# Kernel tuning notes

Measured on AMD Instinct MI355X. Metric: run time of the kernel, lower is better.

Reference implementation:

```python
import jax, jax.numpy as jnp
import numpy as np

K = 5            # self.k
MARGIN_CB = 0.05  # neighborhood_ranking_crossbrain default margin
MARGIN_NRC = 0.4  # self.margin used in partial_nrc_loss
MAX_PAIRS = 6
EPS = 1e-8


def _norm(x):
    return x / jnp.sqrt(jnp.sum(x * x, axis=-1, keepdims=True) + 1e-12)


def _cos_dist_pair(a, b):
    s = jnp.clip(jnp.sum(a * b, axis=-1), -1.0 + EPS, 1.0 - EPS)
    return 1.0 - s


def _pairwise_cos_dist(x, y):
    return 1.0 - _norm(x) @ _norm(y).T


def _sq_dist(x):
    # squared euclidean distance -- same argsort order as torch.cdist
    sq = jnp.sum(x * x, axis=-1)
    return jnp.maximum(sq[:, None] + sq[None, :] - 2.0 * (x @ x.T), 0.0)


def _crossbrain(z1, z2, key):
    # neighborhood_ranking_crossbrain with match_idx = identity (as in forward)
    N = z1.shape[0]
    D1 = jax.lax.stop_gradient(_sq_dist(z1))      # ranking only, no grad
    neigh = jnp.argsort(D1, axis=-1)[:, 1:K + 1]  # (N, K) nearest neighbors
    # sample K distinct negatives per token excluding {n} U neigh[n]:
    scores = jax.random.uniform(key, (N, N))
    rows = jnp.arange(N)
    scores = scores.at[rows[:, None], neigh].set(-jnp.inf)
    scores = scores.at[rows, rows].set(-jnp.inf)
    _, neg = jax.lax.top_k(scores, K)             # (N, K)
    z2n = _norm(z2)
    anchor = z2n[:, None, :]                      # (N,1,C)
    d_pos = _cos_dist_pair(anchor, z2n[neigh])    # (N, K)
    d_neg = _cos_dist_pair(anchor, z2n[neg])      # (N, K)
    return jnp.mean(jax.nn.relu(d_pos - d_neg + MARGIN_CB))


def _nrc_partial(A, B, key):
    # partial_matches_mnn + nrc_on_partial, fully vectorized & masked
    T = A.shape[0]
    D = jax.lax.stop_gradient(_pairwise_cos_dist(A, B))
    b_of_a = jnp.argmin(D, axis=1)
    a_of_b = jnp.argmin(D, axis=0)
    ar = jnp.arange(T)
    mutual = ar == a_of_b[b_of_a]                 # matched A tokens (injective)
    idxB_of_A = jnp.where(mutual, b_of_a, -1)
    is_matched_B = (jnp.zeros(T, jnp.int32).at[b_of_a].add(mutual.astype(jnp.int32)) > 0)
    DA = jax.lax.stop_gradient(_pairwise_cos_dist(A, A))
    neigh = jnp.argsort(DA, axis=-1)[:, 1:K + 1]  # (T, K)
    DB = _pairwise_cos_dist(B, B)                 # grads flow through DB
    posB = idxB_of_A[neigh]                       # (T, K)
    pos_mask = posB >= 0
    # negative pool: unmatched B tokens (stable argsort puts False first)
    order = jnp.argsort(is_matched_B)
    neg_count = jnp.maximum(T - jnp.sum(is_matched_B.astype(jnp.int32)), 1)
    r = jax.random.randint(key, (T, K), 0, T)
    negB = order[r % neg_count]                   # sample with replacement
    uB = jnp.maximum(idxB_of_A, 0)[:, None]
    d_pos = DB[uB, jnp.maximum(posB, 0)]
    d_neg = DB[uB, negB]
    hinge = jax.nn.relu(d_pos - d_neg + MARGIN_NRC) * pos_mask
    per_tok = jnp.sum(hinge, axis=1) / jnp.maximum(jnp.sum(pos_mask, axis=1), 1)
    valid = mutual & jnp.any(pos_mask, axis=1)
    cnt = jnp.sum(valid.astype(jnp.float32))
    return jnp.where(cnt > 0, jnp.sum(per_tok * valid) / jnp.maximum(cnt, 1.0), 0.0)


def _partial_nrc_loss(z1, z2, key, seed):
    Bn = z1.shape[0]
    pairs = [(p, q) for p in range(Bn) for q in range(Bn) if p != q]
    rng = np.random.RandomState(seed)
    if len(pairs) > MAX_PAIRS:
        sel = rng.permutation(len(pairs))[:MAX_PAIRS]
        pairs = [pairs[i] for i in sel]
    ps = jnp.array([p for p, _ in pairs])
    qs = jnp.array([q for _, q in pairs])
    keys = jax.random.split(key, len(pairs))
    losses = jax.vmap(_nrc_partial)(z1[ps], z2[qs], keys)
    return jnp.mean(losses)


def _taco_loss(z1, z2):
    Bn = z1.shape[0]
    base = jax.random.key(42)
    k1, k2, k3, k4 = jax.random.split(base, 4)
    loss2 = (jnp.sum(jax.vmap(_crossbrain)(z1, z2, jax.random.split(k1, Bn)))
             + jnp.sum(jax.vmap(_crossbrain)(z2, z1, jax.random.split(k2, Bn)))) / Bn
    loss3 = _partial_nrc_loss(z1, z2, k3, 0) + _partial_nrc_loss(z2, z1, k4, 1)
    return 10.0 * loss2 + 10.0 * loss3


def setup_inputs() -> dict:
    key = jax.random.key(0)
    k1, k2 = jax.random.split(key)
    Bn, T, C = 4, 2048, 768
    z1 = jax.random.normal(k1, (Bn, T, C), dtype=jnp.float32)
    z2 = jax.random.normal(k2, (Bn, T, C), dtype=jnp.float32)
    return {"z1": z1, "z2": z2}


def reference(z1, z2):
    return _taco_loss(z1, z2)
```

## Files before the change

### kernel.cpp

```cpp
#include <hip/hip_runtime.h>
#include <cstdint>
#include <cstddef>

#define TT 2048
#define CC 768
#define KK 5
#define PCAP 64

typedef __attribute__((ext_vector_type(8))) short short8;
typedef __attribute__((ext_vector_type(4))) short short4v;
typedef __attribute__((ext_vector_type(4))) float float4v;

struct PairTab { int sa[12]; int sb[12]; };
struct PairMap { int src[12]; int tr[12]; };

#define N_SELF_BLK (8 * 136)
#define TP 132

__device__ __forceinline__ unsigned int mix_hash(unsigned int a, unsigned int b) {
  unsigned long long x = (((unsigned long long)a) << 32) | (unsigned long long)b;
  x ^= x >> 33; x *= 0xff51afd7ed558ccdULL;
  x ^= x >> 33; x *= 0xc4ceb9fe1a85ec53ULL;
  x ^= x >> 33;
  return (unsigned int)(x & 0xffffffffu);
}

__device__ __forceinline__ unsigned short f2bf(float x) {
  union { float f; unsigned int u; } v; v.f = x;
  unsigned int r = v.u + 0x7fffu + ((v.u >> 16) & 1u);
  return (unsigned short)(r >> 16);
}

__device__ __forceinline__ float bf2f(unsigned short u) {
  union { unsigned int i; float f; } v; v.i = ((unsigned int)u) << 16; return v.f;
}

__device__ __forceinline__ void gload_lds16(const void* g, void* l) {
  __builtin_amdgcn_global_load_lds(
      (const __attribute__((address_space(1))) unsigned int*)g,
      (__attribute__((address_space(3))) unsigned int*)l, 16, 0, 0);
}

__device__ __forceinline__ bool lexlt(float k1, int i1, float k2, int i2) {
  return k1 < k2 || (k1 == k2 && i1 < i2);
}

#define INS5(kk_, ii_, L)                                                        \
  if (lexlt(kk_, ii_, L##k[4], L##i[4])) {                                       \
    L##k[4] = kk_; L##i[4] = ii_;                                                \
    if (lexlt(L##k[4], L##i[4], L##k[3], L##i[3])) {                             \
      float tk = L##k[3]; int ti_ = L##i[3]; L##k[3] = L##k[4]; L##i[3] = L##i[4]; L##k[4] = tk; L##i[4] = ti_; \
      if (lexlt(L##k[3], L##i[3], L##k[2], L##i[2])) {                           \
        tk = L##k[2]; ti_ = L##i[2]; L##k[2] = L##k[3]; L##i[2] = L##i[3]; L##k[3] = tk; L##i[3] = ti_; \
        if (lexlt(L##k[2], L##i[2], L##k[1], L##i[1])) {                         \
          tk = L##k[1]; ti_ = L##i[1]; L##k[1] = L##k[2]; L##i[1] = L##i[2]; L##k[2] = tk; L##i[2] = ti_; \
          if (lexlt(L##k[1], L##i[1], L##k[0], L##i[0])) {                       \
            tk = L##k[0]; ti_ = L##i[0]; L##k[0] = L##k[1]; L##i[0] = L##i[1]; L##k[1] = tk; L##i[1] = ti_; \
          }                                                                      \
        }                                                                        \
      }                                                                          \
    }                                                                            \
  }

__global__ __launch_bounds__(192) void prep_kernel(const float* __restrict__ z1, const float* __restrict__ z2,
                                                   unsigned short* __restrict__ zb, float* __restrict__ sq,
                                                   float* __restrict__ inv) {
  int r = blockIdx.x;
  const float* p = (r < 4 * TT) ? (z1 + (size_t)r * CC) : (z2 + (size_t)(r - 4 * TT) * CC);
  unsigned short* o = zb + (size_t)r * CC;
  float4 v = ((const float4*)p)[threadIdx.x];
  float s = v.x * v.x + v.y * v.y + v.z * v.z + v.w * v.w;
  ushort4 u;
  u.x = f2bf(v.x); u.y = f2bf(v.y); u.z = f2bf(v.z); u.w = f2bf(v.w);
  ((ushort4*)o)[threadIdx.x] = u;
#pragma unroll
  for (int off = 32; off > 0; off >>= 1) s += __shfl_down(s, off, 64);
  __shared__ float wred[3];
  int lane = threadIdx.x & 63, w = threadIdx.x >> 6;
  if (lane == 0) wred[w] = s;
  __syncthreads();
  if (threadIdx.x == 0) {
    float tot = wred[0] + wred[1] + wred[2];
    sq[r] = tot; inv[r] = rsqrtf(tot + 1e-12f);
  }
}

struct SmemKL { unsigned short As[128 * 64]; unsigned short Bs[128 * 64]; };
union SmemU {
  SmemKL st;
  unsigned short tile[128 * TP];
};

__device__ __forceinline__ void gram_mainloop(const unsigned short* __restrict__ A,
                                              const unsigned short* __restrict__ B,
                                              int bm, int bn, SmemKL& st, float4v (&acc)[4][4]) {
  const int lane = threadIdx.x & 63, waveId = threadIdx.x >> 6;
  const int wm = (waveId >> 1) * 64, wn = (waveId & 1) * 64;
  const int lrow = lane & 15, lquad = lane >> 4;
  for (int kk = 0; kk < CC; kk += 64) {
#pragma unroll
    for (int c = 0; c < 4; ++c) {
      int l = c * 256 + threadIdx.x;
      int row = l >> 3, pc = l & 7;
      int sc = pc ^ (row & 7);
      gload_lds16(A + (size_t)(bm + row) * CC + kk + sc * 8, &st.As[l * 8]);
      gload_lds16(B + (size_t)(bn + row) * CC + kk + sc * 8, &st.Bs[l * 8]);
    }
    __syncthreads();
#pragma unroll
    for (int h = 0; h < 2; ++h) {
      short8 af[4], bfr[4];
#pragma unroll
      for (int i = 0; i < 4; ++i) {
        int ra = wm + i * 16 + lrow;
        int ca = (h * 4 + lquad) ^ (ra & 7);
        af[i] = *(const short8*)&st.As[ra * 64 + ca * 8];
        int rb = wn + i * 16 + lrow;
        int cb2 = (h * 4 + lquad) ^ (rb & 7);
        bfr[i] = *(const short8*)&st.Bs[rb * 64 + cb2 * 8];
      }
#pragma unroll
      for (int i = 0; i < 4; ++i)
#pragma unroll
        for (int j = 0; j < 4; ++j)
          acc[i][j] = __builtin_amdgcn_mfma_f32_16x16x32_bf16(af[i], bfr[j], acc[i][j], 0, 0, 0);
    }
    __syncthreads();
  }
}

__global__ __launch_bounds__(256, 4) void gram_self(const unsigned short* __restrict__ zb,
                                                    unsigned short* __restrict__ gram) {
  __shared__ SmemU sm;
  const int bid = blockIdx.x;
  int s = bid / 136;
  int t = bid % 136;
  int ti = 0;
  while (t >= 16 - ti) { t -= 16 - ti; ++ti; }
  int tj = ti + t;
  int bm = ti * 128, bn = tj * 128;
  const unsigned short* A = zb + (size_t)s * TT * CC;

  float4v acc[4][4];
#pragma unroll
  for (int i = 0; i < 4; ++i)
#pragma unroll
    for (int j = 0; j < 4; ++j) acc[i][j] = (float4v){0.f, 0.f, 0.f, 0.f};

  gram_mainloop(A, A, bm, bn, sm.st, acc);

  const int lane = threadIdx.x & 63, waveId = threadIdx.x >> 6;
  const int wm = (waveId >> 1) * 64, wn = (waveId & 1) * 64;
  const int lrow = lane & 15, lquad = lane >> 4;

#pragma unroll
  for (int i = 0; i < 4; ++i)
#pragma unroll
    for (int j = 0; j < 4; ++j)
#pragma unroll
      for (int r = 0; r < 4; ++r) {
        int lr = wm + i * 16 + lquad * 4 + r;
        int lc = wn + j * 16 + lrow;
        sm.tile[lr * TP + lc] = f2bf(acc[i][j][r]);
      }
  __syncthreads();
  unsigned short* G = gram + (size_t)s * TT * TT;
  for (int it = 0; it < 16; ++it) {
    int task = it * 256 + threadIdx.x;
    int r = task >> 5;
    int c = task & 31;
    short4v v = *(const short4v*)&sm.tile[r * TP + c * 4];
    *(short4v*)&G[(size_t)(bm + r) * TT + bn + c * 4] = v;
  }
  if (bm != bn) {
    for (int it = 0; it < 16; ++it) {
      int task = it * 256 + threadIdx.x;
      int cc = task >> 5;
      int q = task & 31;
      short4v v;
      v[0] = (short)sm.tile[(q * 4 + 0) * TP + cc];
      v[1] = (short)sm.tile[(q * 4 + 1) * TP + cc];
      v[2] = (short)sm.tile[(q * 4 + 2) * TP + cc];
      v[3] = (short)sm.tile[(q * 4 + 3) * TP + cc];
      *(short4v*)&G[(size_t)(bn + cc) * TT + bm + q * 4] = v;
    }
  }
}

__global__ __launch_bounds__(256, 4) void gram_cross(const unsigned short* __restrict__ zb,
                                                     const float* __restrict__ invAll, PairTab tab,
                                                     float* __restrict__ prow_v, int* __restrict__ prow_i,
                                                     float* __restrict__ pcol_v, int* __restrict__ pcol_i) {
  __shared__ SmemKL smk;
  __shared__ float sInvA[128], sInvB[128];
  __shared__ float rowv[2][128]; __shared__ int rowi[2][128];
  __shared__ float colv[2][128]; __shared__ int coli[2][128];

  const int cbid = blockIdx.x;
  const int p = cbid >> 8;
  const int tile = cbid & 255;
  const int bn = (tile & 15) * 128;
  const int bm = (tile >> 4) * 128;
  const unsigned short* A = zb + (size_t)tab.sa[p] * TT * CC;
  const unsigned short* B = zb + (size_t)tab.sb[p] * TT * CC;
  if (threadIdx.x < 128) sInvA[threadIdx.x] = invAll[(size_t)tab.sa[p] * TT + bm + threadIdx.x];
  else sInvB[threadIdx.x - 128] = invAll[(size_t)tab.sb[p] * TT + bn + threadIdx.x - 128];

  float4v acc[4][4];
#pragma unroll
  for (int i = 0; i < 4; ++i)
#pragma unroll
    for (int j = 0; j < 4; ++j) acc[i][j] = (float4v){0.f, 0.f, 0.f, 0.f};

  gram_mainloop(A, B, bm, bn, smk, acc);

  const int lane = threadIdx.x & 63, waveId = threadIdx.x >> 6;
  const int wm = (waveId >> 1) * 64, wn = (waveId & 1) * 64;
  const int lrow = lane & 15, lquad = lane >> 4;

  float rbv[4][4]; int rbi[4][4];
#pragma unroll
  for (int i = 0; i < 4; ++i)
#pragma unroll
    for (int r = 0; r < 4; ++r) { rbv[i][r] = INFINITY; rbi[i][r] = TT; }
#pragma unroll
  for (int i = 0; i < 4; ++i)
#pragma unroll
    for (int j = 0; j < 4; ++j) {
      int col = bn + wn + j * 16 + lrow;
      float ivb = sInvB[wn + j * 16 + lrow];
#pragma unroll
      for (int r = 0; r < 4; ++r) {
        float v = -acc[i][j][r] * ivb;
        if (v < rbv[i][r]) { rbv[i][r] = v; rbi[i][r] = col; }
      }
    }
#pragma unroll
  for (int m = 1; m <= 8; m <<= 1) {
#pragma unroll
    for (int i = 0; i < 4; ++i)
#pragma unroll
      for (int r = 0; r < 4; ++r) {
        float v2 = __shfl_xor(rbv[i][r], m, 64);
        int i2 = __shfl_xor(rbi[i][r], m, 64);
        if (v2 < rbv[i][r] || (v2 == rbv[i][r] && i2 < rbi[i][r])) { rbv[i][r] = v2; rbi[i][r] = i2; }
      }
  }
  if (lrow == 0) {
#pragma unroll
    for (int i = 0; i < 4; ++i)
#pragma unroll
      for (int r = 0; r < 4; ++r) {
        int lr = wm + i * 16 + lquad * 4 + r;
        rowv[wn >> 6][lr] = rbv[i][r]; rowi[wn >> 6][lr] = rbi[i][r];
      }
  }

  float cbv[4]; int cbi[4];
#pragma unroll
  for (int j = 0; j < 4; ++j) { cbv[j] = INFINITY; cbi[j] = TT; }
#pragma unroll
  for (int j = 0; j < 4; ++j)
#pragma unroll
    for (int i = 0; i < 4; ++i)
#pragma unroll
      for (int r = 0; r < 4; ++r) {
        int lr = wm + i * 16 + lquad * 4 + r;
        float v = -acc[i][j][r] * sInvA[lr];
        if (v < cbv[j]) { cbv[j] = v; cbi[j] = bm + lr; }
      }
#pragma unroll
  for (int m = 16; m <= 32; m <<= 1) {
#pragma unroll
    for (int j = 0; j < 4; ++j) {
      float v2 = __shfl_xor(cbv[j], m, 64);
      int i2 = __shfl_xor(cbi[j], m, 64);
      if (v2 < cbv[j] || (v2 == cbv[j] && i2 < cbi[j])) { cbv[j] = v2; cbi[j] = i2; }
    }
  }
  if (lquad == 0) {
#pragma unroll
    for (int j = 0; j < 4; ++j) {
      int lc = wn + j * 16 + lrow;
      colv[wm >> 6][lc] = cbv[j]; coli[wm >> 6][lc] = cbi[j];
    }
  }
  __syncthreads();

  int bj = bn >> 7, bi2 = bm >> 7;
  if (threadIdx.x < 128) {
    int t = threadIdx.x;
    float v0 = rowv[0][t], v1 = rowv[1][t];
    int i0 = rowi[0][t], i1 = rowi[1][t];
    bool take1 = (v1 < v0) || (v1 == v0 && i1 < i0);
    prow_v[((size_t)p * 16 + bj) * TT + bm + t] = take1 ? v1 : v0;
    prow_i[((size_t)p * 16 + bj) * TT + bm + t] = take1 ? i1 : i0;
  } else {
    int t = threadIdx.x - 128;
    float v0 = colv[0][t], v1 = colv[1][t];
    int i0 = coli[0][t], i1 = coli[1][t];
    bool take1 = (v1 < v0) || (v1 == v0 && i1 < i0);
    pcol_v[((size_t)p * 16 + bi2) * TT + bn + t] = take1 ? v1 : v0;
    pcol_i[((size_t)p * 16 + bi2) * TT + bn + t] = take1 ? i1 : i0;
  }
}

__device__ void top5_row_full(const unsigned short* __restrict__ G, const float* __restrict__ sq,
                              const float* __restrict__ inv, int i, int lane,
                              int* __restrict__ o0, int* __restrict__ o1) {
  float ak[5]; int ai[5];
  float bk[5]; int bi[5];
#pragma unroll
  for (int t = 0; t < 5; ++t) { ak[t] = INFINITY; ai[t] = TT; bk[t] = INFINITY; bi[t] = TT; }
#pragma unroll
  for (int step = 0; step < 8; ++step) {
    int j4 = (step * 64 + lane) * 4;
    ushort4 g4u = *(const ushort4*)&G[j4];
    float4 s4 = *(const float4*)&sq[j4];
    float4 v4 = *(const float4*)&inv[j4];
#pragma unroll
    for (int c = 0; c < 4; ++c) {
      int j = j4 + c;
      float g = bf2f((c == 0) ? g4u.x : (c == 1) ? g4u.y : (c == 2) ? g4u.z : g4u.w);
      float sv = (c == 0) ? s4.x : (c == 1) ? s4.y : (c == 2) ? s4.z : s4.w;
      float iv = (c == 0) ? v4.x : (c == 1) ? v4.y : (c == 2) ? v4.z : v4.w;
      float k0 = (j == i) ? INFINITY : sv - 2.f * g;
      float k1 = (j == i) ? INFINITY : -g * iv;
      INS5(k0, j, a)
      INS5(k1, j, b)
    }
  }
#pragma unroll
  for (int m = 1; m <= 32; m <<= 1) {
    float ok[5]; int oi[5];
#pragma unroll
    for (int t = 0; t < 5; ++t) { ok[t] = __shfl_xor(ak[t], m, 64); oi[t] = __shfl_xor(ai[t], m, 64); }
#pragma unroll
    for (int t = 0; t < 5; ++t) { INS5(ok[t], oi[t], a) }
#pragma unroll
    for (int t = 0; t < 5; ++t) { ok[t] = __shfl_xor(bk[t], m, 64); oi[t] = __shfl_xor(bi[t], m, 64); }
#pragma unroll
    for (int t = 0; t < 5; ++t) { INS5(ok[t], oi[t], b) }
  }
  if (lane < KK) {
    int v0 = (lane == 0) ? ai[0] : (lane == 1) ? ai[1] : (lane == 2) ? ai[2] : (lane == 3) ? ai[3] : ai[4];
    int v1 = (lane == 0) ? bi[0] : (lane == 1) ? bi[1] : (lane == 2) ? bi[2] : (lane == 3) ? bi[3] : bi[4];
    o0[lane] = v0;
    o1[lane] = v1;
  }
}

__global__ __launch_bounds__(256) void top5_batched(const unsigned short* __restrict__ gram,
                                                    const float* __restrict__ sqAll,
                                                    const float* __restrict__ invAll,
                                                    int* __restrict__ out0, int* __restrict__ out1) {
  int s = blockIdx.y;
  int w = threadIdx.x >> 6, lane = threadIdx.x & 63;
  int i = blockIdx.x * 4 + w;
  const unsigned short* G = gram + (size_t)s * TT * TT + (size_t)i * TT;
  const float* sq = sqAll + (size_t)s * TT;
  const float* inv = invAll + (size_t)s * TT;

  __shared__ float pvv[4][2][PCAP];
  __shared__ int pix[4][2][PCAP];
  __shared__ int pcnt[4][2];
  if (lane < 2) pcnt[w][lane] = 0;

  float mn0 = INFINITY, mn1 = INFINITY;
#pragma unroll
  for (int step = 0; step < 8; ++step) {
    int j4 = (step * 64 + lane) * 4;
    ushort4 g4u = *(const ushort4*)&G[j4];
    float4 s4 = *(const float4*)&sq[j4];
    float4 v4 = *(const float4*)&inv[j4];
#pragma unroll
    for (int c = 0; c < 4; ++c) {
      int j = j4 + c;
      float g = bf2f((c == 0) ? g4u.x : (c == 1) ? g4u.y : (c == 2) ? g4u.z : g4u.w);
      float sv = (c == 0) ? s4.x : (c == 1) ? s4.y : (c == 2) ? s4.z : s4.w;
      float iv = (c == 0) ? v4.x : (c == 1) ? v4.y : (c == 2) ? v4.z : v4.w;
      float k0 = (j == i) ? INFINITY : sv - 2.f * g;
      float k1 = (j == i) ? INFINITY : -g * iv;
      mn0 = fminf(mn0, k0);
      mn1 = fminf(mn1, k1);
    }
  }
#pragma unroll
  for (int m = 1; m <= 4; m <<= 1) {
    mn0 = fminf(mn0, __shfl_xor(mn0, m, 64));
    mn1 = fminf(mn1, __shfl_xor(mn1, m, 64));
  }
  float gv0[8], gv1[8];
#pragma unroll
  for (int g = 0; g < 8; ++g) {
    gv0[g] = __shfl(mn0, g * 8, 64);
    gv1[g] = __shfl(mn1, g * 8, 64);
  }
  float T0 = 0.f, T1 = 0.f;
#pragma unroll
  for (int g = 0; g < 8; ++g) {
    int r0 = 0, r1 = 0;
#pragma unroll
    for (int h = 0; h < 8; ++h) {
      r0 += ((gv0[h] < gv0[g]) || (gv0[h] == gv0[g] && h < g)) ? 1 : 0;
      r1 += ((gv1[h] < gv1[g]) || (gv1[h] == gv1[g] && h < g)) ? 1 : 0;
    }
    if (r0 == 4) T0 = gv0[g];
    if (r1 == 4) T1 = gv1[g];
  }

#pragma unroll
  for (int step = 0; step < 8; ++step) {
    int j4 = (step * 64 + lane) * 4;
    ushort4 g4u = *(const ushort4*)&G[j4];
    float4 s4 = *(const float4*)&sq[j4];
    float4 v4 = *(const float4*)&inv[j4];
#pragma unroll
    for (int c = 0; c < 4; ++c) {
      int j = j4 + c;
      float g = bf2f((c == 0) ? g4u.x : (c == 1) ? g4u.y : (c == 2) ? g4u.z : g4u.w);
      float sv = (c == 0) ? s4.x : (c == 1) ? s4.y : (c == 2) ? s4.z : s4.w;
      float iv = (c == 0) ? v4.x : (c == 1) ? v4.y : (c == 2) ? v4.z : v4.w;
      float k0 = (j == i) ? INFINITY : sv - 2.f * g;
      float k1 = (j == i) ? INFINITY : -g * iv;
      bool c0 = (k0 <= T0), c1 = (k1 <= T1);
      if (__any(c0)) {
        if (c0) {
          int q = atomicAdd(&pcnt[w][0], 1);
          if (q < PCAP) { pvv[w][0][q] = k0; pix[w][0][q] = j; }
        }
      }
      if (__any(c1)) {
        if (c1) {
          int q = atomicAdd(&pcnt[w][1], 1);
          if (q < PCAP) { pvv[w][1][q] = k1; pix[w][1][q] = j; }
        }
      }
    }
  }

  int c0n = pcnt[w][0], c1n = pcnt[w][1];
  if (c0n > PCAP || c1n > PCAP) {
    top5_row_full(G, sq, inv, i, lane,
                  out0 + ((size_t)s * TT + i) * KK, out1 + ((size_t)s * TT + i) * KK);
    return;
  }
  {
    float cv = (lane < c0n) ? pvv[w][0][lane] : INFINITY;
    int ci = (lane < c0n) ? pix[w][0][lane] : TT;
    int r = 0;
    for (int t = 0; t < c0n; ++t) {
      float ov = pvv[w][0][t]; int oi = pix[w][0][t];
      r += lexlt(ov, oi, cv, ci) ? 1 : 0;
    }
    if (lane < c0n && r < KK) out0[((size_t)s * TT + i) * KK + r] = ci;
  }
  {
    float cv = (lane < c1n) ? pvv[w][1][lane] : INFINITY;
    int ci = (lane < c1n) ? pix[w][1][lane] : TT;
    int r = 0;
    for (int t = 0; t < c1n; ++t) {
      float ov = pvv[w][1][t]; int oi = pix[w][1][t];
      r += lexlt(ov, oi, cv, ci) ? 1 : 0;
    }
    if (lane < c1n && r < KK) out1[((size_t)s * TT + i) * KK + r] = ci;
  }
}

__device__ void argmin_body(int bx, int p, const float* __restrict__ prow_v, const int* __restrict__ prow_i,
                            const float* __restrict__ pcol_v, const int* __restrict__ pcol_i,
                            const PairMap& pm,
                            int* __restrict__ b_of_a, int* __restrict__ a_of_b) {
  int u = pm.src[p];
  bool tr = pm.tr[p] != 0;
  int t = bx * 256 + threadIdx.x;
  int isRow = t < TT;
  int x = isRow ? t : t - TT;
  bool useRow = (isRow != 0) != tr;
  const float* pv = (useRow ? prow_v : pcol_v) + (size_t)u * 16 * TT;
  const int* pi = (useRow ? prow_i : pcol_i) + (size_t)u * 16 * TT;
  float best = INFINITY; int bidx = TT;
  for (int s = 0; s < 16; ++s) {
    float v = pv[(size_t)s * TT + x]; int id = pi[(size_t)s * TT + x];
    if (v < best || (v == best && id < bidx)) { best = v; bidx = id; }
  }
  if (isRow) b_of_a[(size_t)p * TT + x] = bidx;
  else       a_of_b[(size_t)p * TT + x] = bidx;
}

__device__ void cb_hinge_body(int bx, int c, const unsigned short* __restrict__ gram, const float* __restrict__ invAll,
                              const int* __restrict__ neigh1, float* __restrict__ cb_acc) {
  int i0 = bx * 64;
  int sa = c, sb = (c < 4) ? (c + 4) : (c - 4);
  const unsigned short* Gs = gram + (size_t)sb * TT * TT;
  const float* invB = invAll + (size_t)sb * TT;
  const int* neighA = neigh1 + (size_t)sa * TT * KK;
  unsigned int seed = 0x13579BDFu + 0x9E3779B9u * (unsigned)c;
  int tid = threadIdx.x;

  __shared__ int targ[64][10];
  __shared__ float sval[64][10];
  for (int t = tid; t < 64 * KK; t += 256) targ[t / KK][t % KK] = neighA[(size_t)i0 * KK + t];
  __syncthreads();
  if (tid < 64) {
    int i = i0 + tid;
    int pos[KK];
#pragma unroll
    for (int k = 0; k < KK; ++k) pos[k] = targ[tid][k];
    unsigned int ctr = 0;
    for (int k = 0; k < KK; ++k) {
      int cand;
      while (true) {
        unsigned int h = mix_hash(seed ^ (unsigned)i, ctr++);
        cand = (int)(h & (TT - 1));
        bool bad = (cand == i);
        for (int t = 0; t < KK; ++t) bad = bad || (cand == pos[t]);
        for (int t = 0; t < k; ++t) bad = bad || (cand == targ[tid][KK + t]);
        if (!bad) break;
      }
      targ[tid][KK + k] = cand;
    }
  }
  __syncthreads();
  for (int t = tid; t < 640; t += 256) {
    int il = t / 10, k = t % 10;
    int tt = targ[il][k];
    sval[il][k] = bf2f(Gs[(size_t)(i0 + il) * TT + tt]) * invB[tt];
  }
  __syncthreads();
  if (tid < 64) {
    int i = i0 + tid;
    float ii = invB[i];
    const float lo = -1.f + 1e-8f, hi = 1.f - 1e-8f;
    float hsum = 0.f;
#pragma unroll
    for (int k = 0; k < KK; ++k) {
      float sp = fminf(fmaxf(sval[tid][k] * ii, lo), hi);
      float sn = fminf(fmaxf(sval[tid][KK + k] * ii, lo), hi);
      float h = sn - sp + 0.05f;
      hsum += (h > 0.f) ? h : 0.f;
    }
#pragma unroll
    for (int off = 32; off > 0; off >>= 1) hsum += __shfl_down(hsum, off, 64);
    if (tid == 0) atomicAdd(&cb_acc[c], hsum);
  }
}

__global__ __launch_bounds__(256) void cb_argmin_fused(const unsigned short* __restrict__ gram,
                                                       const float* __restrict__ invAll,
                                                       const int* __restrict__ neigh1, float* __restrict__ cb_acc,
                                                       const float* __restrict__ prow_v, const int* __restrict__ prow_i,
                                                       const float* __restrict__ pcol_v, const int* __restrict__ pcol_i,
                                                       PairMap pm,
                                                       int* __restrict__ b_of_a, int* __restrict__ a_of_b) {
  unsigned int b = blockIdx.x;
  if (b < 256) {
    cb_hinge_body((int)(b & 31), (int)(b >> 5), gram, invAll, neigh1, cb_acc);
  } else {
    unsigned int t = b - 256;
    argmin_body((int)(t & 15), (int)(t >> 4), prow_v, prow_i, pcol_v, pcol_i, pm, b_of_a, a_of_b);
  }
}

__global__ __launch_bounds__(256) void mutual_batched(const int* __restrict__ b_of_a_all,
                                                      const int* __restrict__ a_of_b_all,
                                                      int* __restrict__ idxB_all, int* __restrict__ matchedB_all,
                                                      int* __restrict__ unmatched_all, int* __restrict__ scalars_all) {
  int p = blockIdx.x;
  const int* b_of_a = b_of_a_all + (size_t)p * TT;
  const int* a_of_b = a_of_b_all + (size_t)p * TT;
  int* idxB_of_A = idxB_all + (size_t)p * TT;
  int* matchedB = matchedB_all + (size_t)p * TT;
  int* unmatched = unmatched_all + (size_t)p * TT;
  __shared__ int cnt_sh;
  for (int j = threadIdx.x; j < TT; j += 256) matchedB[j] = 0;
  __syncthreads();
  for (int i = threadIdx.x; i < TT; i += 256) {
    int b = b_of_a[i];
    bool mut = (a_of_b[b] == i);
    idxB_of_A[i] = mut ? b : -1;
    if (mut) matchedB[b] = 1;
  }
  __syncthreads();
  if (threadIdx.x == 0) cnt_sh = 0;
  __syncthreads();
  for (int j = threadIdx.x; j < TT; j += 256) {
    if (!matchedB[j]) { int q = atomicAdd(&cnt_sh, 1); unmatched[q] = j; }
  }
  __syncthreads();
  if (threadIdx.x == 0) {
    int c = cnt_sh;
    if (c == 0) { unmatched[0] = 0; c = 1; }
    scalars_all[p * 16] = c;
  }
}

__global__ __launch_bounds__(256) void nrc_hinge_block(const unsigned short* __restrict__ gram, const float* __restrict__ invAll,
                                                       const int* __restrict__ neighC, const int* __restrict__ idxB_all,
                                                       const int* __restrict__ unmatched_all,
                                                       const int* __restrict__ scalars_all,
                                                       PairTab tab, float* __restrict__ nrc_acc) {
  int p = blockIdx.y;
  int i0 = blockIdx.x * 64;
  int sa = tab.sa[p], sb = tab.sb[p];
  const unsigned short* Gs = gram + (size_t)sb * TT * TT;
  const float* invB = invAll + (size_t)sb * TT;
  const int* neighA = neighC + (size_t)sa * TT * KK;
  const int* idxB_of_A = idxB_all + (size_t)p * TT;
  const int* unmatched = unmatched_all + (size_t)p * TT;
  unsigned int seed = 0xC0FFEE11u + 0x9E3779B9u * (unsigned)p;
  float* acc = nrc_acc + p * 2;
  int tid = threadIdx.x;

  __shared__ int targ[64][10];
  __shared__ float sval[64][10];
  __shared__ unsigned int tmask[64];
  __shared__ int su[64];
  if (tid < 64) { tmask[tid] = 0; su[tid] = idxB_of_A[i0 + tid]; }
  __syncthreads();
  unsigned int neg_count = (unsigned int)scalars_all[p * 16];
  for (int t = tid; t < 64 * KK; t += 256) {
    int il = t / KK, k = t % KK;
    int nb = neighA[(size_t)i0 * KK + t];
    int pb = idxB_of_A[nb];
    targ[il][k] = (pb >= 0) ? pb : 0;
    if (pb >= 0) atomicOr(&tmask[il], 1u << k);
  }
  for (int t = tid; t < 64 * KK; t += 256) {
    int il = t / KK, k = t % KK;
    int i = i0 + il;
    unsigned int r = mix_hash(seed ^ 0xA5A5u, (unsigned)(i * KK + k)) & (TT - 1);
    targ[il][KK + k] = unmatched[r % neg_count];
  }
  __syncthreads();
  for (int t = tid; t < 640; t += 256) {
    int il = t / 10, k = t % 10;
    int u = su[il] >= 0 ? su[il] : 0;
    int tt = targ[il][k];
    sval[il][k] = bf2f(Gs[(size_t)u * TT + tt]) * invB[tt];
  }
  __syncthreads();
  if (tid < 64) {
    int idx = su[tid];
    int u = idx >= 0 ? idx : 0;
    float iu = invB[u];
    unsigned int tm = tmask[tid];
    float hsum = 0.f; int pcnt = 0;
#pragma unroll
    for (int k = 0; k < KK; ++k) {
      if (tm & (1u << k)) {
        float dpos = 1.f - sval[tid][k] * iu;
        float dneg = 1.f - sval[tid][KK + k] * iu;
        float h = dpos - dneg + 0.4f;
        hsum += (h > 0.f) ? h : 0.f;
        pcnt++;
      }
    }
    float hs = 0.f, vc = 0.f;
    if (idx >= 0 && pcnt > 0) { hs = hsum / (float)pcnt; vc = 1.0f; }
#pragma unroll
    for (int off = 32; off > 0; off >>= 1) {
      hs += __shfl_down(hs, off, 64);
      vc += __shfl_down(vc, off, 64);
    }
    if (tid == 0) {
      atomicAdd(&acc[0], hs);
      atomicAdd(&acc[1], vc);
    }
  }
}

__global__ void final_kernel(const float* __restrict__ cb_acc, const float* __restrict__ nrc_acc,
                             float* __restrict__ out) {
  float loss2 = 0.f;
  for (int c = 0; c < 8; ++c) loss2 += cb_acc[c] * (1.0f / 10240.0f);
  loss2 *= 0.25f;
  float loss3 = 0.f;
  for (int d = 0; d < 2; ++d) {
    float s = 0.f;
    for (int t = 0; t < 6; ++t) {
      float cnt = nrc_acc[(d * 6 + t) * 2 + 1];
      float sum = nrc_acc[(d * 6 + t) * 2 + 0];
      s += (cnt > 0.f) ? (sum / cnt) : 0.f;
    }
    loss3 += s * (1.f / 6.f);
  }
  out[0] = 10.f * loss2 + 10.f * loss3;
}

namespace {
struct MT19937 {
  uint32_t mt[624]; int mti;
  void seed(uint32_t s) {
    mt[0] = s;
    for (int i = 1; i < 624; ++i) mt[i] = 1812433253u * (mt[i - 1] ^ (mt[i - 1] >> 30)) + (uint32_t)i;
    mti = 624;
  }
  uint32_t next() {
    if (mti >= 624) {
      for (int i = 0; i < 624; ++i) {
        uint32_t y = (mt[i] & 0x80000000u) | (mt[(i + 1) % 624] & 0x7fffffffu);
        uint32_t v = y >> 1;
        if (y & 1u) v ^= 0x9908b0dfu;
        mt[i] = mt[(i + 397) % 624] ^ v;
      }
      mti = 0;
    }
    uint32_t y = mt[mti++];
    y ^= y >> 11; y ^= (y << 7) & 0x9d2c5680u; y ^= (y << 15) & 0xefc60000u; y ^= y >> 18;
    return y;
  }
  uint32_t interval(uint32_t mx) {
    uint32_t mask = mx;
    mask |= mask >> 1; mask |= mask >> 2; mask |= mask >> 4; mask |= mask >> 8; mask |= mask >> 16;
    while (true) { uint32_t v = next() & mask; if (v <= mx) return v; }
  }
};
inline void np_perm12_first6(uint32_t seed, int* sel6) {
  int a[12]; for (int i = 0; i < 12; ++i) a[i] = i;
  MT19937 r; r.seed(seed);
  for (int i = 11; i >= 1; --i) { uint32_t j = r.interval((uint32_t)i); int t = a[i]; a[i] = a[j]; a[j] = t; }
  for (int i = 0; i < 6; ++i) sel6[i] = a[i];
}
}

extern "C" void kernel_launch(void* const* d_in, const int* in_sizes, int n_in,
                              void* d_out, int out_size, void* d_ws, size_t ws_size,
                              hipStream_t stream) {
  const float* z1 = (const float*)d_in[0];
  const float* z2 = (const float*)d_in[1];
  float* out = (float*)d_out;

  char* base = (char*)d_ws;
  size_t off = 0;
  auto alloc = [&](size_t bytes) -> void* {
    void* p = base + off;
    off = (off + bytes + 255) & ~(size_t)255;
    return p;
  };
  unsigned short* gram   = (unsigned short*)alloc((size_t)8 * TT * TT * 2);
  unsigned short* zb     = (unsigned short*)alloc((size_t)8 * TT * CC * 2);
  float* sq              = (float*)alloc((size_t)8 * TT * 4);
  float* inv             = (float*)alloc((size_t)8 * TT * 4);
  int*   neigh1          = (int*)alloc((size_t)8 * TT * KK * 4);
  int*   neighC          = (int*)alloc((size_t)8 * TT * KK * 4);
  float* prow_v          = (float*)alloc((size_t)12 * 16 * TT * 4);
  int*   prow_i          = (int*)alloc((size_t)12 * 16 * TT * 4);
  float* pcol_v          = (float*)alloc((size_t)12 * 16 * TT * 4);
  int*   pcol_i          = (int*)alloc((size_t)12 * 16 * TT * 4);
  int*   b_of_a          = (int*)alloc((size_t)12 * TT * 4);
  int*   a_of_b          = (int*)alloc((size_t)12 * TT * 4);
  int*   idxB            = (int*)alloc((size_t)12 * TT * 4);
  int*   matchedB        = (int*)alloc((size_t)12 * TT * 4);
  int*   unmatched       = (int*)alloc((size_t)12 * TT * 4);
  int*   scalars         = (int*)alloc(12 * 16 * 4);
  float* accs            = (float*)alloc(64 * 4);
  float* cb_acc          = accs;
  float* nrc_acc         = accs + 8;

  hipMemsetAsync(accs, 0, 64 * 4, stream);

  int sel0[6], sel1[6];
  np_perm12_first6(0u, sel0);
  np_perm12_first6(1u, sel1);
  static const int PP[12] = {0, 0, 0, 1, 1, 1, 2, 2, 2, 3, 3, 3};
  static const int QQ[12] = {1, 2, 3, 0, 2, 3, 0, 1, 3, 0, 1, 2};
  PairTab tab;
  for (int d = 0; d < 2; ++d) {
    const int* sel = (d == 0) ? sel0 : sel1;
    for (int t = 0; t < 6; ++t) {
      int pi_ = PP[sel[t]], qi = QQ[sel[t]];
      int p = d * 6 + t;
      tab.sa[p] = (d == 0) ? pi_ : 4 + pi_;
      tab.sb[p] = (d == 0) ? 4 + qi : qi;
    }
  }

  PairTab gtab; PairMap pm; int nU = 0;
  for (int p = 0; p < 12; ++p) {
    int f = -1, ftr = 0;
    for (int q = 0; q < nU; ++q) {
      if (gtab.sa[q] == tab.sb[p] && gtab.sb[q] == tab.sa[p]) { f = q; ftr = 1; break; }
      if (gtab.sa[q] == tab.sa[p] && gtab.sb[q] == tab.sb[p]) { f = q; ftr = 0; break; }
    }
    if (f >= 0) { pm.src[p] = f; pm.tr[p] = ftr; }
    else { gtab.sa[nU] = tab.sa[p]; gtab.sb[nU] = tab.sb[p]; pm.src[p] = nU; pm.tr[p] = 0; ++nU; }
  }

  prep_kernel<<<8 * TT, 192, 0, stream>>>(z1, z2, zb, sq, inv);

  gram_self<<<N_SELF_BLK, 256, 0, stream>>>(zb, gram);

  gram_cross<<<nU * 256, 256, 0, stream>>>(zb, inv, gtab, prow_v, prow_i, pcol_v, pcol_i);

  top5_batched<<<dim3(TT / 4, 8), 256, 0, stream>>>(gram, sq, inv, neigh1, neighC);

  cb_argmin_fused<<<256 + 192, 256, 0, stream>>>(gram, inv, neigh1, cb_acc,
                                                 prow_v, prow_i, pcol_v, pcol_i, pm, b_of_a, a_of_b);

  mutual_batched<<<12, 256, 0, stream>>>(b_of_a, a_of_b, idxB, matchedB, unmatched, scalars);
  nrc_hinge_block<<<dim3(TT / 64, 12), 256, 0, stream>>>(gram, inv, neighC, idxB, unmatched, scalars, tab, nrc_acc);

  final_kernel<<<1, 1, 0, stream>>>(cb_acc, nrc_acc, out);
}
```

Before: 314.1 us.

## Merge independent kernels into fused launches and cache gram rows in LDS

Merges gram_self and gram_cross into one launch that dispatches on block index over a shared-memory union. Moves the argmin reduction into the top5 launch and mutual matching into the cb_hinge launch, cutting the pipeline by two kernel launches and letting independent work share the GPU at the same time. top5 also keeps its gram row in LDS so the second pass reads it from there instead of global memory. The added LDS may reduce occupancy, and the union means the cross blocks use as much LDS as the larger self blocks.

```diff
diff --git a/kernel.cpp b/kernel.cpp
--- a/kernel.cpp
+++ b/kernel.cpp
@@ -90,6 +90,13 @@
   SmemKL st;
   unsigned short tile[128 * TP];
 };
+struct CrossSm {
+  SmemKL st;
+  float sInvA[128]; float sInvB[128];
+  float rowv[2][128]; int rowi[2][128];
+  float colv[2][128]; int coli[2][128];
+};
+union GramSm { CrossSm cross; SmemU selfu; };
 
 __device__ __forceinline__ void gram_mainloop(const unsigned short* __restrict__ A,
                                               const unsigned short* __restrict__ B,
@@ -129,10 +136,8 @@
   }
 }
 
-__global__ __launch_bounds__(256, 4) void gram_self(const unsigned short* __restrict__ zb,
-                                                    unsigned short* __restrict__ gram) {
-  __shared__ SmemU sm;
-  const int bid = blockIdx.x;
+__device__ void gram_self_body(int bid, const unsigned short* __restrict__ zb,
+                               unsigned short* __restrict__ gram, SmemU& sm) {
   int s = bid / 136;
   int t = bid % 136;
   int ti = 0;
@@ -187,24 +192,19 @@
   }
 }
 
-__global__ __launch_bounds__(256, 4) void gram_cross(const unsigned short* __restrict__ zb,
-                                                     const float* __restrict__ invAll, PairTab tab,
-                                                     float* __restrict__ prow_v, int* __restrict__ prow_i,
-                                                     float* __restrict__ pcol_v, int* __restrict__ pcol_i) {
-  __shared__ SmemKL smk;
-  __shared__ float sInvA[128], sInvB[128];
-  __shared__ float rowv[2][128]; __shared__ int rowi[2][128];
-  __shared__ float colv[2][128]; __shared__ int coli[2][128];
-
-  const int cbid = blockIdx.x;
+__device__ void gram_cross_body(int cbid, const unsigned short* __restrict__ zb,
+                                const float* __restrict__ invAll, const PairTab& tab,
+                                float* __restrict__ prow_v, int* __restrict__ prow_i,
+                                float* __restrict__ pcol_v, int* __restrict__ pcol_i,
+                                CrossSm& cs) {
   const int p = cbid >> 8;
   const int tile = cbid & 255;
   const int bn = (tile & 15) * 128;
   const int bm = (tile >> 4) * 128;
   const unsigned short* A = zb + (size_t)tab.sa[p] * TT * CC;
   const unsigned short* B = zb + (size_t)tab.sb[p] * TT * CC;
-  if (threadIdx.x < 128) sInvA[threadIdx.x] = invAll[(size_t)tab.sa[p] * TT + bm + threadIdx.x];
-  else sInvB[threadIdx.x - 128] = invAll[(size_t)tab.sb[p] * TT + bn + threadIdx.x - 128];
+  if (threadIdx.x < 128) cs.sInvA[threadIdx.x] = invAll[(size_t)tab.sa[p] * TT + bm + threadIdx.x];
+  else cs.sInvB[threadIdx.x - 128] = invAll[(size_t)tab.sb[p] * TT + bn + threadIdx.x - 128];
 
   float4v acc[4][4];
 #pragma unroll
@@ -212,7 +212,7 @@
 #pragma unroll
     for (int j = 0; j < 4; ++j) acc[i][j] = (float4v){0.f, 0.f, 0.f, 0.f};
 
-  gram_mainloop(A, B, bm, bn, smk, acc);
+  gram_mainloop(A, B, bm, bn, cs.st, acc);
 
   const int lane = threadIdx.x & 63, waveId = threadIdx.x >> 6;
   const int wm = (waveId >> 1) * 64, wn = (waveId & 1) * 64;
@@ -228,7 +228,7 @@
 #pragma unroll
     for (int j = 0; j < 4; ++j) {
       int col = bn + wn + j * 16 + lrow;
-      float ivb = sInvB[wn + j * 16 + lrow];
+      float ivb = cs.sInvB[wn + j * 16 + lrow];
 #pragma unroll
       for (int r = 0; r < 4; ++r) {
         float v = -acc[i][j][r] * ivb;
@@ -252,7 +252,7 @@
 #pragma unroll
       for (int r = 0; r < 4; ++r) {
         int lr = wm + i * 16 + lquad * 4 + r;
-        rowv[wn >> 6][lr] = rbv[i][r]; rowi[wn >> 6][lr] = rbi[i][r];
+        cs.rowv[wn >> 6][lr] = rbv[i][r]; cs.rowi[wn >> 6][lr] = rbi[i][r];
       }
   }
 
@@ -266,7 +266,7 @@
 #pragma unroll
       for (int r = 0; r < 4; ++r) {
         int lr = wm + i * 16 + lquad * 4 + r;
-        float v = -acc[i][j][r] * sInvA[lr];
+        float v = -acc[i][j][r] * cs.sInvA[lr];
         if (v < cbv[j]) { cbv[j] = v; cbi[j] = bm + lr; }
       }
 #pragma unroll
@@ -282,7 +282,7 @@
 #pragma unroll
     for (int j = 0; j < 4; ++j) {
       int lc = wn + j * 16 + lrow;
-      colv[wm >> 6][lc] = cbv[j]; coli[wm >> 6][lc] = cbi[j];
+      cs.colv[wm >> 6][lc] = cbv[j]; cs.coli[wm >> 6][lc] = cbi[j];
     }
   }
   __syncthreads();
@@ -290,18 +290,33 @@
   int bj = bn >> 7, bi2 = bm >> 7;
   if (threadIdx.x < 128) {
     int t = threadIdx.x;
-    float v0 = rowv[0][t], v1 = rowv[1][t];
-    int i0 = rowi[0][t], i1 = rowi[1][t];
+    float v0 = cs.rowv[0][t], v1 = cs.rowv[1][t];
+    int i0 = cs.rowi[0][t], i1 = cs.rowi[1][t];
     bool take1 = (v1 < v0) || (v1 == v0 && i1 < i0);
     prow_v[((size_t)p * 16 + bj) * TT + bm + t] = take1 ? v1 : v0;
     prow_i[((size_t)p * 16 + bj) * TT + bm + t] = take1 ? i1 : i0;
   } else {
     int t = threadIdx.x - 128;
-    float v0 = colv[0][t], v1 = colv[1][t];
-    int i0 = coli[0][t], i1 = coli[1][t];
+    float v0 = cs.colv[0][t], v1 = cs.colv[1][t];
+    int i0 = cs.coli[0][t], i1 = cs.coli[1][t];
     bool take1 = (v1 < v0) || (v1 == v0 && i1 < i0);
     pcol_v[((size_t)p * 16 + bi2) * TT + bn + t] = take1 ? v1 : v0;
     pcol_i[((size_t)p * 16 + bi2) * TT + bn + t] = take1 ? i1 : i0;
+  }
+}
+
+__global__ __launch_bounds__(256, 4) void gram_fused(unsigned int crossN,
+                                                     const unsigned short* __restrict__ zb,
+                                                     unsigned short* __restrict__ gram,
+                                                     const float* __restrict__ invAll, PairTab tab,
+                                                     float* __restrict__ prow_v, int* __restrict__ prow_i,
+                                                     float* __restrict__ pcol_v, int* __restrict__ pcol_i) {
+  __shared__ GramSm sm;
+  unsigned int b = blockIdx.x;
+  if (b < crossN) {
+    gram_cross_body((int)b, zb, invAll, tab, prow_v, prow_i, pcol_v, pcol_i, sm.cross);
+  } else {
+    gram_self_body((int)(b - crossN), zb, gram, sm.selfu);
   }
 }
 
@@ -350,17 +365,16 @@
   }
 }
 
-__global__ __launch_bounds__(256) void top5_batched(const unsigned short* __restrict__ gram,
-                                                    const float* __restrict__ sqAll,
-                                                    const float* __restrict__ invAll,
-                                                    int* __restrict__ out0, int* __restrict__ out1) {
-  int s = blockIdx.y;
+__device__ void top5_body(int s, int bx, const unsigned short* __restrict__ gram,
+                          const float* __restrict__ sqAll, const float* __restrict__ invAll,
+                          int* __restrict__ out0, int* __restrict__ out1) {
   int w = threadIdx.x >> 6, lane = threadIdx.x & 63;
-  int i = blockIdx.x * 4 + w;
+  int i = bx * 4 + w;
   const unsigned short* G = gram + (size_t)s * TT * TT + (size_t)i * TT;
   const float* sq = sqAll + (size_t)s * TT;
   const float* inv = invAll + (size_t)s * TT;
 
+  __shared__ ushort4 rowc4[4][TT / 4];
   __shared__ float pvv[4][2][PCAP];
   __shared__ int pix[4][2][PCAP];
   __shared__ int pcnt[4][2];
@@ -369,8 +383,10 @@
   float mn0 = INFINITY, mn1 = INFINITY;
 #pragma unroll
   for (int step = 0; step < 8; ++step) {
-    int j4 = (step * 64 + lane) * 4;
+    int jc = step * 64 + lane;
+    int j4 = jc * 4;
     ushort4 g4u = *(const ushort4*)&G[j4];
+    rowc4[w][jc] = g4u;
     float4 s4 = *(const float4*)&sq[j4];
     float4 v4 = *(const float4*)&inv[j4];
 #pragma unroll
@@ -411,8 +427,9 @@
 
 #pragma unroll
   for (int step = 0; step < 8; ++step) {
-    int j4 = (step * 64 + lane) * 4;
-    ushort4 g4u = *(const ushort4*)&G[j4];
+    int jc = step * 64 + lane;
+    int j4 = jc * 4;
+    ushort4 g4u = rowc4[w][jc];
     float4 s4 = *(const float4*)&sq[j4];
     float4 v4 = *(const float4*)&inv[j4];
 #pragma unroll
@@ -488,6 +505,23 @@
   else       a_of_b[(size_t)p * TT + x] = bidx;
 }
 
+__global__ __launch_bounds__(256) void top5_argmin_fused(const unsigned short* __restrict__ gram,
+                                                         const float* __restrict__ sqAll,
+                                                         const float* __restrict__ invAll,
+                                                         int* __restrict__ out0, int* __restrict__ out1,
+                                                         const float* __restrict__ prow_v, const int* __restrict__ prow_i,
+                                                         const float* __restrict__ pcol_v, const int* __restrict__ pcol_i,
+                                                         PairMap pm,
+                                                         int* __restrict__ b_of_a, int* __restrict__ a_of_b) {
+  unsigned int b = blockIdx.x;
+  if (b < 4096) {
+    top5_body((int)(b >> 9), (int)(b & 511), gram, sqAll, invAll, out0, out1);
+  } else {
+    unsigned int t = b - 4096;
+    argmin_body((int)(t & 15), (int)(t >> 4), prow_v, prow_i, pcol_v, pcol_i, pm, b_of_a, a_of_b);
+  }
+}
+
 __device__ void cb_hinge_body(int bx, int c, const unsigned short* __restrict__ gram, const float* __restrict__ invAll,
                               const int* __restrict__ neigh1, float* __restrict__ cb_acc) {
   int i0 = bx * 64;
@@ -546,27 +580,10 @@
   }
 }
 
-__global__ __launch_bounds__(256) void cb_argmin_fused(const unsigned short* __restrict__ gram,
-                                                       const float* __restrict__ invAll,
-                                                       const int* __restrict__ neigh1, float* __restrict__ cb_acc,
-                                                       const float* __restrict__ prow_v, const int* __restrict__ prow_i,
-                                                       const float* __restrict__ pcol_v, const int* __restrict__ pcol_i,
-                                                       PairMap pm,
-                                                       int* __restrict__ b_of_a, int* __restrict__ a_of_b) {
-  unsigned int b = blockIdx.x;
-  if (b < 256) {
-    cb_hinge_body((int)(b & 31), (int)(b >> 5), gram, invAll, neigh1, cb_acc);
-  } else {
-    unsigned int t = b - 256;
-    argmin_body((int)(t & 15), (int)(t >> 4), prow_v, prow_i, pcol_v, pcol_i, pm, b_of_a, a_of_b);
-  }
-}
-
-__global__ __launch_bounds__(256) void mutual_batched(const int* __restrict__ b_of_a_all,
-                                                      const int* __restrict__ a_of_b_all,
-                                                      int* __restrict__ idxB_all, int* __restrict__ matchedB_all,
-                                                      int* __restrict__ unmatched_all, int* __restrict__ scalars_all) {
-  int p = blockIdx.x;
+__device__ void mutual_body(int p, const int* __restrict__ b_of_a_all,
+                            const int* __restrict__ a_of_b_all,
+                            int* __restrict__ idxB_all, int* __restrict__ matchedB_all,
+                            int* __restrict__ unmatched_all, int* __restrict__ scalars_all) {
   const int* b_of_a = b_of_a_all + (size_t)p * TT;
   const int* a_of_b = a_of_b_all + (size_t)p * TT;
   int* idxB_of_A = idxB_all + (size_t)p * TT;
@@ -592,6 +609,20 @@
     int c = cnt_sh;
     if (c == 0) { unmatched[0] = 0; c = 1; }
     scalars_all[p * 16] = c;
+  }
+}
+
+__global__ __launch_bounds__(256) void cb_mutual_fused(const unsigned short* __restrict__ gram,
+                                                       const float* __restrict__ invAll,
+                                                       const int* __restrict__ neigh1, float* __restrict__ cb_acc,
+                                                       const int* __restrict__ b_of_a, const int* __restrict__ a_of_b,
+                                                       int* __restrict__ idxB_all, int* __restrict__ matchedB_all,
+                                                       int* __restrict__ unmatched_all, int* __restrict__ scalars_all) {
+  unsigned int b = blockIdx.x;
+  if (b < 256) {
+    cb_hinge_body((int)(b & 31), (int)(b >> 5), gram, invAll, neigh1, cb_acc);
+  } else {
+    mutual_body((int)(b - 256), b_of_a, a_of_b, idxB_all, matchedB_all, unmatched_all, scalars_all);
   }
 }
 
@@ -789,16 +820,16 @@
 
   prep_kernel<<<8 * TT, 192, 0, stream>>>(z1, z2, zb, sq, inv);
 
-  gram_self<<<N_SELF_BLK, 256, 0, stream>>>(zb, gram);
-
-  gram_cross<<<nU * 256, 256, 0, stream>>>(zb, inv, gtab, prow_v, prow_i, pcol_v, pcol_i);
-
-  top5_batched<<<dim3(TT / 4, 8), 256, 0, stream>>>(gram, sq, inv, neigh1, neighC);
-
-  cb_argmin_fused<<<256 + 192, 256, 0, stream>>>(gram, inv, neigh1, cb_acc,
-                                                 prow_v, prow_i, pcol_v, pcol_i, pm, b_of_a, a_of_b);
-
-  mutual_batched<<<12, 256, 0, stream>>>(b_of_a, a_of_b, idxB, matchedB, unmatched, scalars);
+  unsigned int crossN = (unsigned int)(nU * 256);
+  gram_fused<<<crossN + N_SELF_BLK, 256, 0, stream>>>(crossN, zb, gram, inv, gtab,
+                                                      prow_v, prow_i, pcol_v, pcol_i);
+
+  top5_argmin_fused<<<4096 + 192, 256, 0, stream>>>(gram, sq, inv, neigh1, neighC,
+                                                    prow_v, prow_i, pcol_v, pcol_i, pm, b_of_a, a_of_b);
+
+  cb_mutual_fused<<<256 + 12, 256, 0, stream>>>(gram, inv, neigh1, cb_acc,
+                                                b_of_a, a_of_b, idxB, matchedB, unmatched, scalars);
+
   nrc_hinge_block<<<dim3(TT / 64, 12), 256, 0, stream>>>(gram, inv, neighC, idxB, unmatched, scalars, tab, nrc_acc);
 
   final_kernel<<<1, 1, 0, stream>>>(cb_acc, nrc_acc, out);
```

After: 389.4 us. 1.24x slower.

## Regroup kernels to cut launches and cache gram row in LDS for top5

Applied to the files above, without the earlier changes.

The argmin blocks move from the cb-hinge kernel into the top5 kernel, and the mutual-match kernel is merged with the cb-hinge kernel, so one launch is removed and the independent small workloads share a grid. The top5 pass also keeps each bf16 gram row in shared memory during the first pass, so the second threshold pass reads LDS instead of reloading the row from global memory. The cost is 16KB more shared memory per top5 block, which may lower occupancy.

```diff
diff --git a/kernel.cpp b/kernel.cpp
--- a/kernel.cpp
+++ b/kernel.cpp
@@ -350,17 +350,16 @@
   }
 }
 
-__global__ __launch_bounds__(256) void top5_batched(const unsigned short* __restrict__ gram,
-                                                    const float* __restrict__ sqAll,
-                                                    const float* __restrict__ invAll,
-                                                    int* __restrict__ out0, int* __restrict__ out1) {
-  int s = blockIdx.y;
+__device__ void top5_body(int s, int bx, const unsigned short* __restrict__ gram,
+                          const float* __restrict__ sqAll, const float* __restrict__ invAll,
+                          int* __restrict__ out0, int* __restrict__ out1) {
   int w = threadIdx.x >> 6, lane = threadIdx.x & 63;
-  int i = blockIdx.x * 4 + w;
+  int i = bx * 4 + w;
   const unsigned short* G = gram + (size_t)s * TT * TT + (size_t)i * TT;
   const float* sq = sqAll + (size_t)s * TT;
   const float* inv = invAll + (size_t)s * TT;
 
+  __shared__ ushort4 rowc4[4][TT / 4];
   __shared__ float pvv[4][2][PCAP];
   __shared__ int pix[4][2][PCAP];
   __shared__ int pcnt[4][2];
@@ -369,8 +368,10 @@
   float mn0 = INFINITY, mn1 = INFINITY;
 #pragma unroll
   for (int step = 0; step < 8; ++step) {
-    int j4 = (step * 64 + lane) * 4;
+    int jc = step * 64 + lane;
+    int j4 = jc * 4;
     ushort4 g4u = *(const ushort4*)&G[j4];
+    rowc4[w][jc] = g4u;
     float4 s4 = *(const float4*)&sq[j4];
     float4 v4 = *(const float4*)&inv[j4];
 #pragma unroll
@@ -411,8 +412,9 @@
 
 #pragma unroll
   for (int step = 0; step < 8; ++step) {
-    int j4 = (step * 64 + lane) * 4;
-    ushort4 g4u = *(const ushort4*)&G[j4];
+    int jc = step * 64 + lane;
+    int j4 = jc * 4;
+    ushort4 g4u = rowc4[w][jc];
     float4 s4 = *(const float4*)&sq[j4];
     float4 v4 = *(const float4*)&inv[j4];
 #pragma unroll
@@ -488,6 +490,23 @@
   else       a_of_b[(size_t)p * TT + x] = bidx;
 }
 
+__global__ __launch_bounds__(256) void top5_argmin_fused(const unsigned short* __restrict__ gram,
+                                                         const float* __restrict__ sqAll,
+                                                         const float* __restrict__ invAll,
+                                                         int* __restrict__ out0, int* __restrict__ out1,
+                                                         const float* __restrict__ prow_v, const int* __restrict__ prow_i,
+                                                         const float* __restrict__ pcol_v, const int* __restrict__ pcol_i,
+                                                         PairMap pm,
+                                                         int* __restrict__ b_of_a, int* __restrict__ a_of_b) {
+  unsigned int b = blockIdx.x;
+  if (b < 4096) {
+    top5_body((int)(b >> 9), (int)(b & 511), gram, sqAll, invAll, out0, out1);
+  } else {
+    unsigned int t = b - 4096;
+    argmin_body((int)(t & 15), (int)(t >> 4), prow_v, prow_i, pcol_v, pcol_i, pm, b_of_a, a_of_b);
+  }
+}
+
 __device__ void cb_hinge_body(int bx, int c, const unsigned short* __restrict__ gram, const float* __restrict__ invAll,
                               const int* __restrict__ neigh1, float* __restrict__ cb_acc) {
   int i0 = bx * 64;
@@ -546,27 +565,10 @@
   }
 }
 
-__global__ __launch_bounds__(256) void cb_argmin_fused(const unsigned short* __restrict__ gram,
-                                                       const float* __restrict__ invAll,
-                                                       const int* __restrict__ neigh1, float* __restrict__ cb_acc,
-                                                       const float* __restrict__ prow_v, const int* __restrict__ prow_i,
-                                                       const float* __restrict__ pcol_v, const int* __restrict__ pcol_i,
-                                                       PairMap pm,
-                                                       int* __restrict__ b_of_a, int* __restrict__ a_of_b) {
-  unsigned int b = blockIdx.x;
-  if (b < 256) {
-    cb_hinge_body((int)(b & 31), (int)(b >> 5), gram, invAll, neigh1, cb_acc);
-  } else {
-    unsigned int t = b - 256;
-    argmin_body((int)(t & 15), (int)(t >> 4), prow_v, prow_i, pcol_v, pcol_i, pm, b_of_a, a_of_b);
-  }
-}
-
-__global__ __launch_bounds__(256) void mutual_batched(const int* __restrict__ b_of_a_all,
-                                                      const int* __restrict__ a_of_b_all,
-                                                      int* __restrict__ idxB_all, int* __restrict__ matchedB_all,
-                                                      int* __restrict__ unmatched_all, int* __restrict__ scalars_all) {
-  int p = blockIdx.x;
+__device__ void mutual_body(int p, const int* __restrict__ b_of_a_all,
+                            const int* __restrict__ a_of_b_all,
+                            int* __restrict__ idxB_all, int* __restrict__ matchedB_all,
+                            int* __restrict__ unmatched_all, int* __restrict__ scalars_all) {
   const int* b_of_a = b_of_a_all + (size_t)p * TT;
   const int* a_of_b = a_of_b_all + (size_t)p * TT;
   int* idxB_of_A = idxB_all + (size_t)p * TT;
@@ -592,6 +594,20 @@
     int c = cnt_sh;
     if (c == 0) { unmatched[0] = 0; c = 1; }
     scalars_all[p * 16] = c;
+  }
+}
+
+__global__ __launch_bounds__(256) void cb_mutual_fused(const unsigned short* __restrict__ gram,
+                                                       const float* __restrict__ invAll,
+                                                       const int* __restrict__ neigh1, float* __restrict__ cb_acc,
+                                                       const int* __restrict__ b_of_a, const int* __restrict__ a_of_b,
+                                                       int* __restrict__ idxB_all, int* __restrict__ matchedB_all,
+                                                       int* __restrict__ unmatched_all, int* __restrict__ scalars_all) {
+  unsigned int b = blockIdx.x;
+  if (b < 256) {
+    cb_hinge_body((int)(b & 31), (int)(b >> 5), gram, invAll, neigh1, cb_acc);
+  } else {
+    mutual_body((int)(b - 256), b_of_a, a_of_b, idxB_all, matchedB_all, unmatched_all, scalars_all);
   }
 }
 
@@ -793,12 +809,12 @@
 
   gram_cross<<<nU * 256, 256, 0, stream>>>(zb, inv, gtab, prow_v, prow_i, pcol_v, pcol_i);
 
-  top5_batched<<<dim3(TT / 4, 8), 256, 0, stream>>>(gram, sq, inv, neigh1, neighC);
-
-  cb_argmin_fused<<<256 + 192, 256, 0, stream>>>(gram, inv, neigh1, cb_acc,
-                                                 prow_v, prow_i, pcol_v, pcol_i, pm, b_of_a, a_of_b);
-
-  mutual_batched<<<12, 256, 0, stream>>>(b_of_a, a_of_b, idxB, matchedB, unmatched, scalars);
+  top5_argmin_fused<<<4096 + 192, 256, 0, stream>>>(gram, sq, inv, neigh1, neighC,
+                                                    prow_v, prow_i, pcol_v, pcol_i, pm, b_of_a, a_of_b);
+
+  cb_mutual_fused<<<256 + 12, 256, 0, stream>>>(gram, inv, neigh1, cb_acc,
+                                                b_of_a, a_of_b, idxB, matchedB, unmatched, scalars);
+
   nrc_hinge_block<<<dim3(TT / 64, 12), 256, 0, stream>>>(gram, inv, neighC, idxB, unmatched, scalars, tab, nrc_acc);
 
   final_kernel<<<1, 1, 0, stream>>>(cb_acc, nrc_acc, out);
```

New measurement: 300.7 us. 4.3% less time.
